# Optimization experiments

Hardware: AMD Instinct MI355X
Metric: run time of the kernel (lower is better)

## Reference

```python
import jax, jax.numpy as jnp
import numpy as np

B, SQ, SK, D, H = 4, 2048, 2048, 1024, 16
HD = D // H
SCALE = HD ** -0.5


def setup_inputs() -> dict:
    key = jax.random.key(0)
    ks = jax.random.split(key, 11)
    s = 0.02
    return {
        "query": jax.random.normal(ks[0], (B, SQ, D), jnp.float32),
        "key": jax.random.normal(ks[1], (B, SK, D), jnp.float32),
        "value": jax.random.normal(ks[2], (B, SK, D), jnp.float32),
        "Wq": jax.random.normal(ks[3], (D, D), jnp.float32) * s,
        "bq": jnp.zeros((D,), jnp.float32),
        "Wk": jax.random.normal(ks[4], (D, D), jnp.float32) * s,
        "bk": jnp.zeros((D,), jnp.float32),
        "Wv": jax.random.normal(ks[5], (D, D), jnp.float32) * s,
        "bv": jnp.zeros((D,), jnp.float32),
        "Wo": jax.random.normal(ks[6], (D, D), jnp.float32) * s,
        "bo": jnp.zeros((D,), jnp.float32),
    }


def reference(query, key, value, Wq, bq, Wk, bk, Wv, bv, Wo, bo):
    # Linear projections (torch nn.Linear: x @ W.T + b)
    Q = query @ Wq.T + bq          # (B, SQ, D)
    K = key @ Wk.T + bk            # (B, SK, D)
    V = value @ Wv.T + bv          # (B, SK, D)
    # split heads -> (B, H, S, HD)
    Q = Q.reshape(B, SQ, H, HD).transpose(0, 2, 1, 3)
    K = K.reshape(B, SK, H, HD).transpose(0, 2, 1, 3)
    V = V.reshape(B, SK, H, HD).transpose(0, 2, 1, 3)
    scores = jnp.einsum('bhqd,bhkd->bhqk', Q, K) * SCALE
    attn = jax.nn.softmax(scores, axis=-1)     # (B, H, SQ, SK); dropout=0 (eval)
    attended = jnp.einsum('bhqk,bhkd->bhqd', attn, V)
    attended = attended.mean(axis=1)           # head-average -> (B, SQ, HD)
    attended = jnp.tile(attended, (1, 1, H))   # repeat to (B, SQ, D)
    output = attended @ Wo.T + bo
    avg_attention = attn.mean(axis=1)          # (B, SQ, SK)
    return (output, avg_attention)
```

## Files before the change

kernel.cpp:

```cpp
#include <hip/hip_runtime.h>
#include <hip/hip_bf16.h>
#include <math.h>

#define BB 4
#define SQL 2048
#define SKL 2048
#define DM 1024
#define NH 16
#define HDIM 64
#define QSCALE 0.18033688011112042f

typedef __attribute__((ext_vector_type(8))) short bf16x8;
typedef __attribute__((ext_vector_type(4))) float f32x4;
typedef __attribute__((ext_vector_type(16))) float f32x16;

__device__ __forceinline__ float exp2fast(float x) { return __builtin_amdgcn_exp2f(x); }
__device__ __forceinline__ float log2fast(float x) { return __builtin_amdgcn_logf(x); }

__device__ __forceinline__ unsigned short f2bf(float f) {
    union { __hip_bfloat16 h; unsigned short u; } c;
    c.h = __float2bfloat16(f);
    return c.u;
}

__device__ __forceinline__ unsigned cvtpk(float lo, float hi) {
    unsigned r;
    asm("v_cvt_pk_bf16_f32 %0, %1, %2" : "=v"(r) : "v"(lo), "v"(hi));
    return r;
}

__device__ __forceinline__ bf16x8 cvt8(const float4& a, const float4& b) {
    bf16x8 r;
    r[0] = (short)f2bf(a.x); r[1] = (short)f2bf(a.y);
    r[2] = (short)f2bf(a.z); r[3] = (short)f2bf(a.w);
    r[4] = (short)f2bf(b.x); r[5] = (short)f2bf(b.y);
    r[6] = (short)f2bf(b.z); r[7] = (short)f2bf(b.w);
    return r;
}

__device__ __forceinline__ void gload16(const void* g, void* l) {
    __builtin_amdgcn_global_load_lds(
        (const __attribute__((address_space(1))) unsigned int*)g,
        (__attribute__((address_space(3))) unsigned int*)l, 16, 0, 0);
}

#define VMCNT0() asm volatile("s_waitcnt vmcnt(0)" ::: "memory")

__global__ __launch_bounds__(256)
void wo_eff_kernel(const float* __restrict__ Wo, float* __restrict__ We) {
    int i = blockIdx.x * 256 + threadIdx.x;
    if (i < DM * HDIM) {
        int n = i >> 6, d = i & 63;
        float s = 0.f;
#pragma unroll
        for (int h = 0; h < NH; ++h) s += Wo[(size_t)n * DM + h * HDIM + d];
        We[i] = s;
    }
}

__global__ __launch_bounds__(256)
void proj_bf16(const float* __restrict__ X, const float* __restrict__ W,
               const float* __restrict__ bias, unsigned short* __restrict__ Y,
               float scale)
{
    __shared__ __align__(16) unsigned short As[128 * 32];
    __shared__ __align__(16) unsigned short Bs[128 * 32];
    const int tid = threadIdx.x;
    const int lane = tid & 63, wid = tid >> 6;
    const int g = lane >> 4, lm = lane & 15;
    const int wr = wid >> 1, wc = wid & 1;
    const int m0 = blockIdx.x * 128, n0 = blockIdx.y * 128;

    int rA[2], cA[2], offA[2];
#pragma unroll
    for (int i = 0; i < 2; ++i) {
        int q = tid + i * 256;
        rA[i] = q >> 2; cA[i] = q & 3;
        offA[i] = rA[i] * 32 + ((cA[i] ^ (rA[i] & 3)) << 3);
    }
    float4 xa[2][2], wa[2][2], xb[2][2], wb[2][2];
#pragma unroll
    for (int i = 0; i < 2; ++i) {
        const float* xp = &X[(size_t)(m0 + rA[i]) * DM + cA[i] * 8];
        const float* wp = &W[(size_t)(n0 + rA[i]) * DM + cA[i] * 8];
        xa[i][0] = *(const float4*)xp; xa[i][1] = *(const float4*)(xp + 4);
        wa[i][0] = *(const float4*)wp; wa[i][1] = *(const float4*)(wp + 4);
    }
    const f32x4 fz = {0.f, 0.f, 0.f, 0.f};
    f32x4 acc[4][4];
#pragma unroll
    for (int i = 0; i < 4; ++i)
#pragma unroll
        for (int j = 0; j < 4; ++j) acc[i][j] = fz;

    for (int t = 0; t < 32; ++t) {
        __syncthreads();
#pragma unroll
        for (int i = 0; i < 2; ++i) {
            *(bf16x8*)&As[offA[i]] = cvt8(xa[i][0], xa[i][1]);
            *(bf16x8*)&Bs[offA[i]] = cvt8(wa[i][0], wa[i][1]);
        }
        if (t < 31) {
            int k0 = (t + 1) * 32;
#pragma unroll
            for (int i = 0; i < 2; ++i) {
                const float* xp = &X[(size_t)(m0 + rA[i]) * DM + k0 + cA[i] * 8];
                const float* wp = &W[(size_t)(n0 + rA[i]) * DM + k0 + cA[i] * 8];
                xb[i][0] = *(const float4*)xp; xb[i][1] = *(const float4*)(xp + 4);
                wb[i][0] = *(const float4*)wp; wb[i][1] = *(const float4*)(wp + 4);
            }
        }
        __syncthreads();
        bf16x8 a[4], b[4];
#pragma unroll
        for (int f = 0; f < 4; ++f) {
            int ra = wr * 64 + f * 16 + lm;
            a[f] = *(const bf16x8*)&As[ra * 32 + (((g) ^ (ra & 3)) << 3)];
            int rb = wc * 64 + f * 16 + lm;
            b[f] = *(const bf16x8*)&Bs[rb * 32 + (((g) ^ (rb & 3)) << 3)];
        }
#pragma unroll
        for (int fm = 0; fm < 4; ++fm)
#pragma unroll
            for (int fn = 0; fn < 4; ++fn)
                acc[fm][fn] = __builtin_amdgcn_mfma_f32_16x16x32_bf16(
                    a[fm], b[fn], acc[fm][fn], 0, 0, 0);
        if (t < 31) {
#pragma unroll
            for (int i = 0; i < 2; ++i) {
                xa[i][0] = xb[i][0]; xa[i][1] = xb[i][1];
                wa[i][0] = wb[i][0]; wa[i][1] = wb[i][1];
            }
        }
    }
    float bn[4];
#pragma unroll
    for (int fn = 0; fn < 4; ++fn) bn[fn] = bias[n0 + wc * 64 + fn * 16 + lm];
#pragma unroll
    for (int fm = 0; fm < 4; ++fm)
#pragma unroll
        for (int i = 0; i < 4; ++i) {
            int m = m0 + wr * 64 + fm * 16 + 4 * g + i;
#pragma unroll
            for (int fn = 0; fn < 4; ++fn) {
                int n = n0 + wc * 64 + fn * 16 + lm;
                Y[(size_t)m * DM + n] = f2bf((acc[fm][fn][i] + bn[fn]) * scale);
            }
        }
}

__global__ __launch_bounds__(256)
void transpose_v(const unsigned short* __restrict__ V, unsigned short* __restrict__ Vt)
{
    __shared__ __align__(16) unsigned short Ts[64][80];
    const int tid = threadIdx.x;
    const int kv0 = blockIdx.x * 64, h = blockIdx.y, b = blockIdx.z;
#pragma unroll
    for (int i = 0; i < 2; ++i) {
        int q = tid + i * 256;
        int r = q >> 3, c = q & 7;
        *(uint4*)&Ts[r][c * 8] =
            *(const uint4*)&V[(size_t)(b * SKL + kv0 + r) * DM + h * HDIM + c * 8];
    }
    __syncthreads();
#pragma unroll
    for (int i = 0; i < 2; ++i) {
        int q = tid + i * 256;
        int d = q >> 3, kc = q & 7;
        union { unsigned short u16[8]; uint4 v; } tw;
#pragma unroll
        for (int e = 0; e < 8; ++e) tw.u16[e] = Ts[kc * 8 + e][d];
        *(uint4*)&Vt[((size_t)(b * NH + h) * HDIM + d) * SKL + kv0 + kc * 8] = tw.v;
    }
}

__global__ __launch_bounds__(256, 2)
void flash_mfma2(const unsigned short* __restrict__ Q,
                 const unsigned short* __restrict__ K,
                 const unsigned short* __restrict__ Vt,
                 float* __restrict__ uw, float* __restrict__ O)
{
    __shared__ __align__(16) unsigned short sK[2][64 * 64];
    __shared__ __align__(16) unsigned short sV[2][64 * 64];
    const int tid = threadIdx.x;
    const int lane = tid & 63, wid = tid >> 6;
    const int l31 = lane & 31, h8 = lane >> 5;
    const int q0 = blockIdx.x * 256, h = blockIdx.y, b = blockIdx.z;
    const int myq0 = q0 + wid * 32 + l31;
    const int myq1 = myq0 + 128;

    bf16x8 qf0[4], qf1[4];
    {
        const unsigned short* qp0 = &Q[(size_t)(b * SQL + myq0) * DM + h * HDIM + h8 * 8];
        const unsigned short* qp1 = &Q[(size_t)(b * SQL + myq1) * DM + h * HDIM + h8 * 8];
#pragma unroll
        for (int c = 0; c < 4; ++c) {
            qf0[c] = *(const bf16x8*)(qp0 + c * 16);
            qf1[c] = *(const bf16x8*)(qp1 + c * 16);
        }
    }

    int rr[2], cc[2];
#pragma unroll
    for (int i = 0; i < 2; ++i) {
        int s = tid + i * 256;
        rr[i] = s >> 3;
        cc[i] = ((s & 7) ^ (rr[i] & 7)) * 8;
    }
    const unsigned short* Kbase = &K[((size_t)b * SKL) * DM + h * HDIM];
    const unsigned short* Vbase = &Vt[((size_t)(b * NH + h) * HDIM) * SKL];

#pragma unroll
    for (int i = 0; i < 2; ++i) {
        gload16(Kbase + (size_t)rr[i] * DM + cc[i], &sK[0][(wid * 64 + i * 256) * 8]);
        gload16(Vbase + (size_t)rr[i] * SKL + cc[i], &sV[0][(wid * 64 + i * 256) * 8]);
    }
    VMCNT0();
    __syncthreads();

    const f32x16 z16 = {0.f};
    f32x16 o00 = z16, o01 = z16, o10 = z16, o11 = z16;
    float l0 = 0.f, l1 = 0.f;
    int cur = 0;

    for (int kt = 0; kt < SKL / 64; ++kt) {
        if (kt + 1 < SKL / 64) {
            int k0 = (kt + 1) * 64;
#pragma unroll
            for (int i = 0; i < 2; ++i) {
                gload16(Kbase + (size_t)(k0 + rr[i]) * DM + cc[i],
                        &sK[cur ^ 1][(wid * 64 + i * 256) * 8]);
                gload16(Vbase + (size_t)rr[i] * SKL + k0 + cc[i],
                        &sV[cur ^ 1][(wid * 64 + i * 256) * 8]);
            }
        }
        f32x16 c00 = z16, c01 = z16, c10 = z16, c11 = z16;
        __builtin_amdgcn_s_setprio(1);
#pragma unroll
        for (int c = 0; c < 4; ++c) {
            int cg = 2 * c + h8;
            bf16x8 a0 = *(const bf16x8*)&sK[cur][l31 * 64 + ((cg ^ (l31 & 7)) << 3)];
            bf16x8 a1 = *(const bf16x8*)&sK[cur][(32 + l31) * 64 + ((cg ^ (l31 & 7)) << 3)];
            c00 = __builtin_amdgcn_mfma_f32_32x32x16_bf16(a0, qf0[c], c00, 0, 0, 0);
            c01 = __builtin_amdgcn_mfma_f32_32x32x16_bf16(a1, qf0[c], c01, 0, 0, 0);
            c10 = __builtin_amdgcn_mfma_f32_32x32x16_bf16(a0, qf1[c], c10, 0, 0, 0);
            c11 = __builtin_amdgcn_mfma_f32_32x32x16_bf16(a1, qf1[c], c11, 0, 0, 0);
        }
        __builtin_amdgcn_s_setprio(0);
        bf16x8 ap0[4], ap1[4];
        {
            float ps = 0.f;
#pragma unroll
            for (int r = 0; r < 16; ++r) { c00[r] = exp2fast(c00[r]); ps += c00[r]; }
#pragma unroll
            for (int r = 0; r < 16; ++r) { c01[r] = exp2fast(c01[r]); ps += c01[r]; }
            ps += __shfl_xor(ps, 32);
            l0 += ps;
#pragma unroll
            for (int ks = 0; ks < 4; ++ks) {
                const int base = (ks & 1) * 8;
                const f32x16& ct = (ks & 2) ? c01 : c00;
                unsigned wA0 = cvtpk(ct[base + 0], ct[base + 1]);
                unsigned wA1 = cvtpk(ct[base + 2], ct[base + 3]);
                unsigned wB0 = cvtpk(ct[base + 4], ct[base + 5]);
                unsigned wB1 = cvtpk(ct[base + 6], ct[base + 7]);
                asm volatile("v_permlane32_swap_b32 %0, %1" : "+v"(wA0), "+v"(wB0));
                asm volatile("v_permlane32_swap_b32 %0, %1" : "+v"(wA1), "+v"(wB1));
                union { unsigned u[4]; bf16x8 v; } pu;
                pu.u[0] = wA0; pu.u[1] = wA1; pu.u[2] = wB0; pu.u[3] = wB1;
                ap0[ks] = pu.v;
            }
        }
        {
            float ps = 0.f;
#pragma unroll
            for (int r = 0; r < 16; ++r) { c10[r] = exp2fast(c10[r]); ps += c10[r]; }
#pragma unroll
            for (int r = 0; r < 16; ++r) { c11[r] = exp2fast(c11[r]); ps += c11[r]; }
            ps += __shfl_xor(ps, 32);
            l1 += ps;
#pragma unroll
            for (int ks = 0; ks < 4; ++ks) {
                const int base = (ks & 1) * 8;
                const f32x16& ct = (ks & 2) ? c11 : c10;
                unsigned wA0 = cvtpk(ct[base + 0], ct[base + 1]);
                unsigned wA1 = cvtpk(ct[base + 2], ct[base + 3]);
                unsigned wB0 = cvtpk(ct[base + 4], ct[base + 5]);
                unsigned wB1 = cvtpk(ct[base + 6], ct[base + 7]);
                asm volatile("v_permlane32_swap_b32 %0, %1" : "+v"(wA0), "+v"(wB0));
                asm volatile("v_permlane32_swap_b32 %0, %1" : "+v"(wA1), "+v"(wB1));
                union { unsigned u[4]; bf16x8 v; } pu;
                pu.u[0] = wA0; pu.u[1] = wA1; pu.u[2] = wB0; pu.u[3] = wB1;
                ap1[ks] = pu.v;
            }
        }
        __builtin_amdgcn_s_setprio(1);
#pragma unroll
        for (int ks = 0; ks < 4; ++ks) {
            int cg = 2 * ks + h8;
            bf16x8 v0 = *(const bf16x8*)&sV[cur][l31 * 64 + ((cg ^ (l31 & 7)) << 3)];
            bf16x8 v1 = *(const bf16x8*)&sV[cur][(32 + l31) * 64 + ((cg ^ (l31 & 7)) << 3)];
            o00 = __builtin_amdgcn_mfma_f32_32x32x16_bf16(v0, ap0[ks], o00, 0, 0, 0);
            o01 = __builtin_amdgcn_mfma_f32_32x32x16_bf16(v1, ap0[ks], o01, 0, 0, 0);
            o10 = __builtin_amdgcn_mfma_f32_32x32x16_bf16(v0, ap1[ks], o10, 0, 0, 0);
            o11 = __builtin_amdgcn_mfma_f32_32x32x16_bf16(v1, ap1[ks], o11, 0, 0, 0);
        }
        __builtin_amdgcn_s_setprio(0);
        VMCNT0();
        __syncthreads();
        cur ^= 1;
    }

    if (h8 == 0) {
        uw[(size_t)(b * NH + h) * SQL + myq0] = log2fast(l0 * (float)NH);
        uw[(size_t)(b * NH + h) * SQL + myq1] = log2fast(l1 * (float)NH);
    }
    const float inv0 = 1.0f / (l0 * (float)NH);
    const float inv1 = 1.0f / (l1 * (float)NH);
    float* Op0 = &O[((size_t)(b * NH + h) * SQL + myq0) * HDIM];
    float* Op1 = &O[((size_t)(b * NH + h) * SQL + myq1) * HDIM];
#pragma unroll
    for (int i2 = 0; i2 < 4; ++i2) {
        float4 w0, w1;
        int d = 8 * i2 + 4 * h8;
        w0.x = o00[4 * i2 + 0] * inv0; w0.y = o00[4 * i2 + 1] * inv0;
        w0.z = o00[4 * i2 + 2] * inv0; w0.w = o00[4 * i2 + 3] * inv0;
        w1.x = o01[4 * i2 + 0] * inv0; w1.y = o01[4 * i2 + 1] * inv0;
        w1.z = o01[4 * i2 + 2] * inv0; w1.w = o01[4 * i2 + 3] * inv0;
        *(float4*)(Op0 + d) = w0;
        *(float4*)(Op0 + d + 32) = w1;
        w0.x = o10[4 * i2 + 0] * inv1; w0.y = o10[4 * i2 + 1] * inv1;
        w0.z = o10[4 * i2 + 2] * inv1; w0.w = o10[4 * i2 + 3] * inv1;
        w1.x = o11[4 * i2 + 0] * inv1; w1.y = o11[4 * i2 + 1] * inv1;
        w1.z = o11[4 * i2 + 2] * inv1; w1.w = o11[4 * i2 + 3] * inv1;
        *(float4*)(Op1 + d) = w0;
        *(float4*)(Op1 + d + 32) = w1;
    }
}

__global__ __launch_bounds__(256)
void am_reduce(const float* __restrict__ O, float* __restrict__ am)
{
    int i = blockIdx.x * 256 + threadIdx.x;
    int bq = i >> 4, c = i & 15;
    int b = bq >> 11, q = bq & 2047;
    const float* base = O + ((size_t)b * NH * SQL + q) * HDIM + c * 4;
    float4 s = {0.f, 0.f, 0.f, 0.f};
    for (int h = 0; h < NH; ++h) {
        float4 v = *(const float4*)(base + (size_t)h * SQL * HDIM);
        s.x += v.x; s.y += v.y; s.z += v.z; s.w += v.w;
    }
    *(float4*)(am + (size_t)bq * HDIM + c * 4) = s;
}

__global__ __launch_bounds__(512)
void avg_mfma2(const unsigned short* __restrict__ Q, const unsigned short* __restrict__ K,
               const float* __restrict__ uw, float* __restrict__ avg)
{
    __shared__ __align__(16) unsigned short sQ[2][128 * 64];
    __shared__ __align__(16) unsigned short sK[2][128 * 64];
    __shared__ float uS[NH][128];
    const int tid = threadIdx.x;
    const int lane = tid & 63, wid = tid >> 6;
    const int g = lane >> 4, lm = lane & 15;
    const int wq = wid >> 1, wk = wid & 1;
    const int k0 = blockIdx.x * 128, q0 = blockIdx.y * 128, b = blockIdx.z;

    for (int i = tid; i < NH * 128; i += 512) {
        int hh = i >> 7, qq = i & 127;
        uS[hh][qq] = uw[(size_t)(b * NH + hh) * SQL + q0 + qq];
    }

    int rs[2], cs[2];
#pragma unroll
    for (int i = 0; i < 2; ++i) {
        int s = tid + i * 512;
        rs[i] = s >> 3;
        cs[i] = (s & 7) ^ (rs[i] & 7);
    }
    const unsigned short* Qbase = &Q[(size_t)(b * SQL + q0) * DM];
    const unsigned short* Kbase = &K[(size_t)(b * SKL + k0) * DM];
#pragma unroll
    for (int i = 0; i < 2; ++i) {
        gload16(Qbase + (size_t)rs[i] * DM + cs[i] * 8, &sQ[0][(tid + i * 512) * 8]);
        gload16(Kbase + (size_t)rs[i] * DM + cs[i] * 8, &sK[0][(tid + i * 512) * 8]);
    }
    VMCNT0();
    __syncthreads();

    const f32x4 fz = {0.f, 0.f, 0.f, 0.f};
    f32x4 acc[2][4];
#pragma unroll
    for (int mf = 0; mf < 2; ++mf)
#pragma unroll
        for (int nf = 0; nf < 4; ++nf) acc[mf][nf] = fz;

    int cur = 0;
    for (int hh = 0; hh < NH; ++hh) {
        if (hh + 1 < NH) {
#pragma unroll
            for (int i = 0; i < 2; ++i) {
                gload16(Qbase + (size_t)rs[i] * DM + (hh + 1) * HDIM + cs[i] * 8,
                        &sQ[cur ^ 1][(tid + i * 512) * 8]);
                gload16(Kbase + (size_t)rs[i] * DM + (hh + 1) * HDIM + cs[i] * 8,
                        &sK[cur ^ 1][(tid + i * 512) * 8]);
            }
        }
        f32x4 s[2][4];
#pragma unroll
        for (int mf = 0; mf < 2; ++mf)
#pragma unroll
            for (int nf = 0; nf < 4; ++nf) s[mf][nf] = fz;
        __builtin_amdgcn_s_setprio(1);
#pragma unroll
        for (int kk = 0; kk < 2; ++kk) {
            bf16x8 a[2];
#pragma unroll
            for (int mf = 0; mf < 2; ++mf) {
                int ra = wq * 32 + mf * 16 + lm;
                a[mf] = *(const bf16x8*)&sQ[cur][ra * 64 + (((kk * 4 + g) ^ (ra & 7)) << 3)];
            }
#pragma unroll
            for (int nf = 0; nf < 4; ++nf) {
                int rb = wk * 64 + nf * 16 + lm;
                bf16x8 kb = *(const bf16x8*)&sK[cur][rb * 64 + (((kk * 4 + g) ^ (rb & 7)) << 3)];
#pragma unroll
                for (int mf = 0; mf < 2; ++mf)
                    s[mf][nf] = __builtin_amdgcn_mfma_f32_16x16x32_bf16(
                        a[mf], kb, s[mf][nf], 0, 0, 0);
            }
        }
        __builtin_amdgcn_s_setprio(0);
#pragma unroll
        for (int mf = 0; mf < 2; ++mf)
#pragma unroll
            for (int i4 = 0; i4 < 4; ++i4) {
                float u = uS[hh][wq * 32 + mf * 16 + 4 * g + i4];
#pragma unroll
                for (int nf = 0; nf < 4; ++nf)
                    acc[mf][nf][i4] += exp2fast(s[mf][nf][i4] - u);
            }
        VMCNT0();
        __syncthreads();
        cur ^= 1;
    }
#pragma unroll
    for (int mf = 0; mf < 2; ++mf)
#pragma unroll
        for (int i4 = 0; i4 < 4; ++i4) {
            int qrow = q0 + wq * 32 + mf * 16 + 4 * g + i4;
#pragma unroll
            for (int nf = 0; nf < 4; ++nf)
                avg[(size_t)(b * SQL + qrow) * SKL + k0 + wk * 64 + nf * 16 + lm] =
                    acc[mf][nf][i4];
        }
}

__global__ __launch_bounds__(256)
void out_gemm(const float* __restrict__ amp, const float* __restrict__ We,
              const float* __restrict__ bo, float* __restrict__ out)
{
    __shared__ float As[64][68];
    __shared__ float Bs[64][68];
    const int m0 = blockIdx.x << 6, n0 = blockIdx.y << 6;
    const int tid = threadIdx.x;
    const int tx = tid & 15, ty = tid >> 4;
    const int lrow = tid >> 4, ldc = (tid & 15) << 2;
#pragma unroll
    for (int rr = 0; rr < 4; ++rr) {
        int r = (rr << 4) + lrow;
        float4 a = *reinterpret_cast<const float4*>(&amp[(size_t)(m0 + r) * HDIM + ldc]);
        float4 w = *reinterpret_cast<const float4*>(&We[(size_t)(n0 + r) * HDIM + ldc]);
        As[ldc + 0][r] = a.x; As[ldc + 1][r] = a.y; As[ldc + 2][r] = a.z; As[ldc + 3][r] = a.w;
        Bs[ldc + 0][r] = w.x; Bs[ldc + 1][r] = w.y; Bs[ldc + 2][r] = w.z; Bs[ldc + 3][r] = w.w;
    }
    __syncthreads();
    float acc[4][4] = {};
    for (int d = 0; d < 64; ++d) {
        float4 av = *reinterpret_cast<const float4*>(&As[d][ty << 2]);
        float4 bv = *reinterpret_cast<const float4*>(&Bs[d][tx << 2]);
        float aa[4] = {av.x, av.y, av.z, av.w};
        float bb[4] = {bv.x, bv.y, bv.z, bv.w};
#pragma unroll
        for (int i = 0; i < 4; ++i)
#pragma unroll
            for (int j = 0; j < 4; ++j)
                acc[i][j] = fmaf(aa[i], bb[j], acc[i][j]);
    }
    float4 bv = *reinterpret_cast<const float4*>(&bo[n0 + (tx << 2)]);
    float bb4[4] = {bv.x, bv.y, bv.z, bv.w};
#pragma unroll
    for (int i = 0; i < 4; ++i) {
        int m = m0 + (ty << 2) + i;
        float4 o = make_float4(acc[i][0] + bb4[0], acc[i][1] + bb4[1],
                               acc[i][2] + bb4[2], acc[i][3] + bb4[3]);
        *reinterpret_cast<float4*>(&out[(size_t)m * DM + n0 + (tx << 2)]) = o;
    }
}

extern "C" void kernel_launch(void* const* d_in, const int* in_sizes, int n_in,
                              void* d_out, int out_size, void* d_ws, size_t ws_size,
                              hipStream_t stream)
{
    const float* query = (const float*)d_in[0];
    const float* key   = (const float*)d_in[1];
    const float* value = (const float*)d_in[2];
    const float* Wq = (const float*)d_in[3];
    const float* bq = (const float*)d_in[4];
    const float* Wk = (const float*)d_in[5];
    const float* bk = (const float*)d_in[6];
    const float* Wv = (const float*)d_in[7];
    const float* bv = (const float*)d_in[8];
    const float* Wo = (const float*)d_in[9];
    const float* bo = (const float*)d_in[10];

    float* out0 = (float*)d_out;
    float* out_avg = out0 + (size_t)BB * SQL * DM;

    const size_t nQ = (size_t)BB * SQL * DM;
    const size_t nML = (size_t)BB * NH * SQL;
    const size_t nAM = (size_t)BB * SQL * HDIM;
    unsigned short* Qb = (unsigned short*)d_ws;
    unsigned short* Kb = Qb + nQ;
    unsigned short* Vb = Kb + nQ;
    unsigned short* Vt = Vb + nQ;
    float* Ob  = (float*)(Vt + nQ);
    float* uw  = Ob + (size_t)BB * NH * SQL * HDIM;
    float* amb = uw + nML;
    float* We  = amb + nAM;

    dim3 blk(256);
    wo_eff_kernel<<<dim3((DM * HDIM + 255) / 256), blk, 0, stream>>>(Wo, We);

    dim3 gp(64, 8);
    proj_bf16<<<gp, blk, 0, stream>>>(query, Wq, bq, Qb, QSCALE);
    proj_bf16<<<gp, blk, 0, stream>>>(key,   Wk, bk, Kb, 1.0f);
    proj_bf16<<<gp, blk, 0, stream>>>(value, Wv, bv, Vb, 1.0f);

    transpose_v<<<dim3(32, 16, 4), blk, 0, stream>>>(Vb, Vt);
    flash_mfma2<<<dim3(SQL / 256, NH, BB), blk, 0, stream>>>(Qb, Kb, Vt, uw, Ob);
    am_reduce<<<dim3(512), blk, 0, stream>>>(Ob, amb);
    avg_mfma2<<<dim3(SKL / 128, SQL / 128, BB), dim3(512), 0, stream>>>(Qb, Kb, uw, out_avg);
    out_gemm<<<dim3(128, 16), blk, 0, stream>>>(amb, We, bo, out0);
}
```

Baseline: 303.9 us.

## Split flash attention over two KV halves and combine partials in reduction

The flash kernel now launches twice as many blocks, each covering half of the key/value sequence. Each block writes its unnormalized partial output and row sum, using the avg_attention output buffer as scratch. A new small kernel adds the partial sums and computes the log normalizer and its reciprocal. am_reduce then sums both partials with per-head weights. The aim is more parallelism and shorter per-block loops, at the cost of double the partial-output memory traffic and an extra kernel launch.

```diff
diff --git a/kernel.cpp b/kernel.cpp
--- a/kernel.cpp
+++ b/kernel.cpp
@@ -8,6 +8,7 @@
 #define DM 1024
 #define NH 16
 #define HDIM 64
+#define NSPLIT 2
 #define QSCALE 0.18033688011112042f
 
 typedef __attribute__((ext_vector_type(8))) short bf16x8;
@@ -178,16 +179,20 @@
 void flash_mfma2(const unsigned short* __restrict__ Q,
                  const unsigned short* __restrict__ K,
                  const unsigned short* __restrict__ Vt,
-                 float* __restrict__ uw, float* __restrict__ O)
+                 float* __restrict__ lpart, float* __restrict__ Opart)
 {
     __shared__ __align__(16) unsigned short sK[2][64 * 64];
     __shared__ __align__(16) unsigned short sV[2][64 * 64];
     const int tid = threadIdx.x;
     const int lane = tid & 63, wid = tid >> 6;
     const int l31 = lane & 31, h8 = lane >> 5;
-    const int q0 = blockIdx.x * 256, h = blockIdx.y, b = blockIdx.z;
+    const int split = blockIdx.x & (NSPLIT - 1);
+    const int q0 = (blockIdx.x >> 1) * 256;
+    const int h = blockIdx.y, b = blockIdx.z;
     const int myq0 = q0 + wid * 32 + l31;
     const int myq1 = myq0 + 128;
+    const int NT = SKL / 64 / NSPLIT;
+    const int kt0 = split * NT;
 
     bf16x8 qf0[4], qf1[4];
     {
@@ -207,8 +212,8 @@
         rr[i] = s >> 3;
         cc[i] = ((s & 7) ^ (rr[i] & 7)) * 8;
     }
-    const unsigned short* Kbase = &K[((size_t)b * SKL) * DM + h * HDIM];
-    const unsigned short* Vbase = &Vt[((size_t)(b * NH + h) * HDIM) * SKL];
+    const unsigned short* Kbase = &K[((size_t)b * SKL + kt0 * 64) * DM + h * HDIM];
+    const unsigned short* Vbase = &Vt[((size_t)(b * NH + h) * HDIM) * SKL + kt0 * 64];
 
 #pragma unroll
     for (int i = 0; i < 2; ++i) {
@@ -223,8 +228,8 @@
     float l0 = 0.f, l1 = 0.f;
     int cur = 0;
 
-    for (int kt = 0; kt < SKL / 64; ++kt) {
-        if (kt + 1 < SKL / 64) {
+    for (int kt = 0; kt < NT; ++kt) {
+        if (kt + 1 < NT) {
             int k0 = (kt + 1) * 64;
 #pragma unroll
             for (int i = 0; i < 2; ++i) {
@@ -311,44 +316,61 @@
         cur ^= 1;
     }
 
+    const size_t sb = (size_t)(split * BB + b);
     if (h8 == 0) {
-        uw[(size_t)(b * NH + h) * SQL + myq0] = log2fast(l0 * (float)NH);
-        uw[(size_t)(b * NH + h) * SQL + myq1] = log2fast(l1 * (float)NH);
-    }
-    const float inv0 = 1.0f / (l0 * (float)NH);
-    const float inv1 = 1.0f / (l1 * (float)NH);
-    float* Op0 = &O[((size_t)(b * NH + h) * SQL + myq0) * HDIM];
-    float* Op1 = &O[((size_t)(b * NH + h) * SQL + myq1) * HDIM];
+        lpart[(sb * NH + h) * SQL + myq0] = l0;
+        lpart[(sb * NH + h) * SQL + myq1] = l1;
+    }
+    float* Op0 = &Opart[((sb * NH + h) * SQL + myq0) * HDIM];
+    float* Op1 = &Opart[((sb * NH + h) * SQL + myq1) * HDIM];
 #pragma unroll
     for (int i2 = 0; i2 < 4; ++i2) {
         float4 w0, w1;
         int d = 8 * i2 + 4 * h8;
-        w0.x = o00[4 * i2 + 0] * inv0; w0.y = o00[4 * i2 + 1] * inv0;
-        w0.z = o00[4 * i2 + 2] * inv0; w0.w = o00[4 * i2 + 3] * inv0;
-        w1.x = o01[4 * i2 + 0] * inv0; w1.y = o01[4 * i2 + 1] * inv0;
-        w1.z = o01[4 * i2 + 2] * inv0; w1.w = o01[4 * i2 + 3] * inv0;
+        w0.x = o00[4 * i2 + 0]; w0.y = o00[4 * i2 + 1];
+        w0.z = o00[4 * i2 + 2]; w0.w = o00[4 * i2 + 3];
+        w1.x = o01[4 * i2 + 0]; w1.y = o01[4 * i2 + 1];
+        w1.z = o01[4 * i2 + 2]; w1.w = o01[4 * i2 + 3];
         *(float4*)(Op0 + d) = w0;
         *(float4*)(Op0 + d + 32) = w1;
-        w0.x = o10[4 * i2 + 0] * inv1; w0.y = o10[4 * i2 + 1] * inv1;
-        w0.z = o10[4 * i2 + 2] * inv1; w0.w = o10[4 * i2 + 3] * inv1;
-        w1.x = o11[4 * i2 + 0] * inv1; w1.y = o11[4 * i2 + 1] * inv1;
-        w1.z = o11[4 * i2 + 2] * inv1; w1.w = o11[4 * i2 + 3] * inv1;
+        w0.x = o10[4 * i2 + 0]; w0.y = o10[4 * i2 + 1];
+        w0.z = o10[4 * i2 + 2]; w0.w = o10[4 * i2 + 3];
+        w1.x = o11[4 * i2 + 0]; w1.y = o11[4 * i2 + 1];
+        w1.z = o11[4 * i2 + 2]; w1.w = o11[4 * i2 + 3];
         *(float4*)(Op1 + d) = w0;
         *(float4*)(Op1 + d + 32) = w1;
     }
 }
 
 __global__ __launch_bounds__(256)
-void am_reduce(const float* __restrict__ O, float* __restrict__ am)
+void uw_combine(const float* __restrict__ lpart, float* __restrict__ uw,
+                float* __restrict__ linv)
+{
+    int i = blockIdx.x * 256 + threadIdx.x;
+    float l = lpart[i] + lpart[i + BB * NH * SQL];
+    float ln = l * (float)NH;
+    uw[i] = log2fast(ln);
+    linv[i] = 1.0f / ln;
+}
+
+__global__ __launch_bounds__(256)
+void am_reduce(const float* __restrict__ Opart, const float* __restrict__ linv,
+               float* __restrict__ am)
 {
     int i = blockIdx.x * 256 + threadIdx.x;
     int bq = i >> 4, c = i & 15;
     int b = bq >> 11, q = bq & 2047;
-    const float* base = O + ((size_t)b * NH * SQL + q) * HDIM + c * 4;
+    const float* base = Opart + ((size_t)b * NH * SQL + q) * HDIM + c * 4;
+    const float* il = linv + ((size_t)b * NH) * SQL + q;
+    const size_t soff = (size_t)BB * NH * SQL * HDIM;
     float4 s = {0.f, 0.f, 0.f, 0.f};
     for (int h = 0; h < NH; ++h) {
-        float4 v = *(const float4*)(base + (size_t)h * SQL * HDIM);
-        s.x += v.x; s.y += v.y; s.z += v.z; s.w += v.w;
+        const float* p = base + (size_t)h * SQL * HDIM;
+        float4 v0 = *(const float4*)p;
+        float4 v1 = *(const float4*)(p + soff);
+        float w = il[(size_t)h * SQL];
+        s.x += (v0.x + v1.x) * w; s.y += (v0.y + v1.y) * w;
+        s.z += (v0.z + v1.z) * w; s.w += (v0.w + v1.w) * w;
     }
     *(float4*)(am + (size_t)bq * HDIM + c * 4) = s;
 }
@@ -516,6 +538,7 @@
 
     float* out0 = (float*)d_out;
     float* out_avg = out0 + (size_t)BB * SQL * DM;
+    float* Opart = out_avg;
 
     const size_t nQ = (size_t)BB * SQL * DM;
     const size_t nML = (size_t)BB * NH * SQL;
@@ -524,10 +547,11 @@
     unsigned short* Kb = Qb + nQ;
     unsigned short* Vb = Kb + nQ;
     unsigned short* Vt = Vb + nQ;
-    float* Ob  = (float*)(Vt + nQ);
-    float* uw  = Ob + (size_t)BB * NH * SQL * HDIM;
-    float* amb = uw + nML;
-    float* We  = amb + nAM;
+    float* lpart = (float*)(Vt + nQ);
+    float* uw   = lpart + NSPLIT * nML;
+    float* linv = uw + nML;
+    float* amb  = linv + nML;
+    float* We   = amb + nAM;
 
     dim3 blk(256);
     wo_eff_kernel<<<dim3((DM * HDIM + 255) / 256), blk, 0, stream>>>(Wo, We);
@@ -538,8 +562,9 @@
     proj_bf16<<<gp, blk, 0, stream>>>(value, Wv, bv, Vb, 1.0f);
 
     transpose_v<<<dim3(32, 16, 4), blk, 0, stream>>>(Vb, Vt);
-    flash_mfma2<<<dim3(SQL / 256, NH, BB), blk, 0, stream>>>(Qb, Kb, Vt, uw, Ob);
-    am_reduce<<<dim3(512), blk, 0, stream>>>(Ob, amb);
+    flash_mfma2<<<dim3(SQL / 256 * NSPLIT, NH, BB), blk, 0, stream>>>(Qb, Kb, Vt, lpart, Opart);
+    uw_combine<<<dim3(512), blk, 0, stream>>>(lpart, uw, linv);
+    am_reduce<<<dim3(512), blk, 0, stream>>>(Opart, linv, amb);
     avg_mfma2<<<dim3(SKL / 128, SQL / 128, BB), dim3(512), 0, stream>>>(Qb, Kb, uw, out_avg);
     out_gemm<<<dim3(128, 16), blk, 0, stream>>>(amb, We, bo, out0);
 }
```

After: 308.1 us. Within noise of the previous version (+1.4%).

## Rework avg-attention kernel to keep Q in registers with 32x32 MFMA tiles

Applied to the files above, without the earlier changes.

The head-averaged attention kernel now loads each wave's Q rows straight from global memory into registers, prefetching the next head, and stages only a 64-key K tile in shared memory. It uses 32x32x16 MFMA instructions, so each lane owns one query row, and writes its outputs as float4 stores. Blocks shrink from 512 to 256 threads while the grid doubles along the key dimension. Separately, the flash kernel moves its cross-half row-sum shuffle out of the inner loop and runs it once after the loop. The aim is less LDS traffic and fewer shuffles, at the cost of more global Q reads, since each block now covers only 64 keys.

```diff
diff --git a/kernel.cpp b/kernel.cpp
--- a/kernel.cpp
+++ b/kernel.cpp
@@ -254,7 +254,6 @@
             for (int r = 0; r < 16; ++r) { c00[r] = exp2fast(c00[r]); ps += c00[r]; }
 #pragma unroll
             for (int r = 0; r < 16; ++r) { c01[r] = exp2fast(c01[r]); ps += c01[r]; }
-            ps += __shfl_xor(ps, 32);
             l0 += ps;
 #pragma unroll
             for (int ks = 0; ks < 4; ++ks) {
@@ -277,7 +276,6 @@
             for (int r = 0; r < 16; ++r) { c10[r] = exp2fast(c10[r]); ps += c10[r]; }
 #pragma unroll
             for (int r = 0; r < 16; ++r) { c11[r] = exp2fast(c11[r]); ps += c11[r]; }
-            ps += __shfl_xor(ps, 32);
             l1 += ps;
 #pragma unroll
             for (int ks = 0; ks < 4; ++ks) {
@@ -311,6 +309,8 @@
         cur ^= 1;
     }
 
+    l0 += __shfl_xor(l0, 32);
+    l1 += __shfl_xor(l1, 32);
     if (h8 == 0) {
         uw[(size_t)(b * NH + h) * SQL + myq0] = log2fast(l0 * (float)NH);
         uw[(size_t)(b * NH + h) * SQL + myq1] = log2fast(l1 * (float)NH);
@@ -353,107 +353,91 @@
     *(float4*)(am + (size_t)bq * HDIM + c * 4) = s;
 }
 
-__global__ __launch_bounds__(512)
-void avg_mfma2(const unsigned short* __restrict__ Q, const unsigned short* __restrict__ K,
+__global__ __launch_bounds__(256)
+void avg_mfma3(const unsigned short* __restrict__ Q, const unsigned short* __restrict__ K,
                const float* __restrict__ uw, float* __restrict__ avg)
 {
-    __shared__ __align__(16) unsigned short sQ[2][128 * 64];
-    __shared__ __align__(16) unsigned short sK[2][128 * 64];
+    __shared__ __align__(16) unsigned short sK[2][64 * 64];
     __shared__ float uS[NH][128];
     const int tid = threadIdx.x;
     const int lane = tid & 63, wid = tid >> 6;
-    const int g = lane >> 4, lm = lane & 15;
-    const int wq = wid >> 1, wk = wid & 1;
-    const int k0 = blockIdx.x * 128, q0 = blockIdx.y * 128, b = blockIdx.z;
-
-    for (int i = tid; i < NH * 128; i += 512) {
+    const int l31 = lane & 31, h8 = lane >> 5;
+    const int k0 = blockIdx.x * 64, q0 = blockIdx.y * 128, b = blockIdx.z;
+    const int myq = q0 + wid * 32 + l31;
+
+    for (int i = tid; i < NH * 128; i += 256) {
         int hh = i >> 7, qq = i & 127;
         uS[hh][qq] = uw[(size_t)(b * NH + hh) * SQL + q0 + qq];
     }
 
-    int rs[2], cs[2];
-#pragma unroll
-    for (int i = 0; i < 2; ++i) {
-        int s = tid + i * 512;
-        rs[i] = s >> 3;
-        cs[i] = (s & 7) ^ (rs[i] & 7);
-    }
-    const unsigned short* Qbase = &Q[(size_t)(b * SQL + q0) * DM];
+    int rr[2], cc[2];
+#pragma unroll
+    for (int i = 0; i < 2; ++i) {
+        int s = tid + i * 256;
+        rr[i] = s >> 3;
+        cc[i] = ((s & 7) ^ (rr[i] & 7)) * 8;
+    }
     const unsigned short* Kbase = &K[(size_t)(b * SKL + k0) * DM];
-#pragma unroll
-    for (int i = 0; i < 2; ++i) {
-        gload16(Qbase + (size_t)rs[i] * DM + cs[i] * 8, &sQ[0][(tid + i * 512) * 8]);
-        gload16(Kbase + (size_t)rs[i] * DM + cs[i] * 8, &sK[0][(tid + i * 512) * 8]);
-    }
+    const unsigned short* Qrow = &Q[(size_t)(b * SQL + myq) * DM + h8 * 8];
+
+#pragma unroll
+    for (int i = 0; i < 2; ++i)
+        gload16(Kbase + (size_t)rr[i] * DM + cc[i], &sK[0][(wid * 64 + i * 256) * 8]);
+    bf16x8 qfc[4], qfn[4];
+#pragma unroll
+    for (int c = 0; c < 4; ++c) qfc[c] = *(const bf16x8*)(Qrow + c * 16);
     VMCNT0();
     __syncthreads();
 
-    const f32x4 fz = {0.f, 0.f, 0.f, 0.f};
-    f32x4 acc[2][4];
-#pragma unroll
-    for (int mf = 0; mf < 2; ++mf)
-#pragma unroll
-        for (int nf = 0; nf < 4; ++nf) acc[mf][nf] = fz;
-
+    const f32x16 z16 = {0.f};
+    f32x16 acc0 = z16, acc1 = z16;
     int cur = 0;
+
     for (int hh = 0; hh < NH; ++hh) {
         if (hh + 1 < NH) {
 #pragma unroll
-            for (int i = 0; i < 2; ++i) {
-                gload16(Qbase + (size_t)rs[i] * DM + (hh + 1) * HDIM + cs[i] * 8,
-                        &sQ[cur ^ 1][(tid + i * 512) * 8]);
-                gload16(Kbase + (size_t)rs[i] * DM + (hh + 1) * HDIM + cs[i] * 8,
-                        &sK[cur ^ 1][(tid + i * 512) * 8]);
-            }
-        }
-        f32x4 s[2][4];
-#pragma unroll
-        for (int mf = 0; mf < 2; ++mf)
-#pragma unroll
-            for (int nf = 0; nf < 4; ++nf) s[mf][nf] = fz;
+            for (int i = 0; i < 2; ++i)
+                gload16(Kbase + (size_t)rr[i] * DM + (hh + 1) * HDIM + cc[i],
+                        &sK[cur ^ 1][(wid * 64 + i * 256) * 8]);
+#pragma unroll
+            for (int c = 0; c < 4; ++c)
+                qfn[c] = *(const bf16x8*)(Qrow + (hh + 1) * HDIM + c * 16);
+        }
+        f32x16 s0 = z16, s1 = z16;
         __builtin_amdgcn_s_setprio(1);
 #pragma unroll
-        for (int kk = 0; kk < 2; ++kk) {
-            bf16x8 a[2];
-#pragma unroll
-            for (int mf = 0; mf < 2; ++mf) {
-                int ra = wq * 32 + mf * 16 + lm;
-                a[mf] = *(const bf16x8*)&sQ[cur][ra * 64 + (((kk * 4 + g) ^ (ra & 7)) << 3)];
-            }
-#pragma unroll
-            for (int nf = 0; nf < 4; ++nf) {
-                int rb = wk * 64 + nf * 16 + lm;
-                bf16x8 kb = *(const bf16x8*)&sK[cur][rb * 64 + (((kk * 4 + g) ^ (rb & 7)) << 3)];
-#pragma unroll
-                for (int mf = 0; mf < 2; ++mf)
-                    s[mf][nf] = __builtin_amdgcn_mfma_f32_16x16x32_bf16(
-                        a[mf], kb, s[mf][nf], 0, 0, 0);
-            }
+        for (int c = 0; c < 4; ++c) {
+            int cg = 2 * c + h8;
+            bf16x8 a0 = *(const bf16x8*)&sK[cur][l31 * 64 + ((cg ^ (l31 & 7)) << 3)];
+            bf16x8 a1 = *(const bf16x8*)&sK[cur][(32 + l31) * 64 + ((cg ^ (l31 & 7)) << 3)];
+            s0 = __builtin_amdgcn_mfma_f32_32x32x16_bf16(a0, qfc[c], s0, 0, 0, 0);
+            s1 = __builtin_amdgcn_mfma_f32_32x32x16_bf16(a1, qfc[c], s1, 0, 0, 0);
         }
         __builtin_amdgcn_s_setprio(0);
-#pragma unroll
-        for (int mf = 0; mf < 2; ++mf)
-#pragma unroll
-            for (int i4 = 0; i4 < 4; ++i4) {
-                float u = uS[hh][wq * 32 + mf * 16 + 4 * g + i4];
-#pragma unroll
-                for (int nf = 0; nf < 4; ++nf)
-                    acc[mf][nf][i4] += exp2fast(s[mf][nf][i4] - u);
-            }
+        float u = uS[hh][wid * 32 + l31];
+#pragma unroll
+        for (int r = 0; r < 16; ++r) {
+            acc0[r] += exp2fast(s0[r] - u);
+            acc1[r] += exp2fast(s1[r] - u);
+        }
+        if (hh + 1 < NH) {
+#pragma unroll
+            for (int c = 0; c < 4; ++c) qfc[c] = qfn[c];
+        }
         VMCNT0();
         __syncthreads();
         cur ^= 1;
     }
-#pragma unroll
-    for (int mf = 0; mf < 2; ++mf)
-#pragma unroll
-        for (int i4 = 0; i4 < 4; ++i4) {
-            int qrow = q0 + wq * 32 + mf * 16 + 4 * g + i4;
-#pragma unroll
-            for (int nf = 0; nf < 4; ++nf)
-                avg[(size_t)(b * SQL + qrow) * SKL + k0 + wk * 64 + nf * 16 + lm] =
-                    acc[mf][nf][i4];
-        }
+
+    float* ap = &avg[(size_t)(b * SQL + myq) * SKL + k0];
+#pragma unroll
+    for (int i2 = 0; i2 < 4; ++i2) {
+        int k = 8 * i2 + 4 * h8;
+        float4 w0 = {acc0[4 * i2 + 0], acc0[4 * i2 + 1], acc0[4 * i2 + 2], acc0[4 * i2 + 3]};
+        float4 w1 = {acc1[4 * i2 + 0], acc1[4 * i2 + 1], acc1[4 * i2 + 2], acc1[4 * i2 + 3]};
+        *(float4*)(ap + k) = w0;
+        *(float4*)(ap + k + 32) = w1;
+    }
 }
 
 __global__ __launch_bounds__(256)
@@ -540,6 +524,6 @@
     transpose_v<<<dim3(32, 16, 4), blk, 0, stream>>>(Vb, Vt);
     flash_mfma2<<<dim3(SQL / 256, NH, BB), blk, 0, stream>>>(Qb, Kb, Vt, uw, Ob);
     am_reduce<<<dim3(512), blk, 0, stream>>>(Ob, amb);
-    avg_mfma2<<<dim3(SKL / 128, SQL / 128, BB), dim3(512), 0, stream>>>(Qb, Kb, uw, out_avg);
+    avg_mfma3<<<dim3(SKL / 64, SQL / 128, BB), blk, 0, stream>>>(Qb, Kb, uw, out_avg);
     out_gemm<<<dim3(128, 16), blk, 0, stream>>>(amb, We, bo, out0);
 }
```

New measurement: 326.7 us. +7.5%, slower.
